# Optimization experiments

Measured on AMD Instinct MI355X. Metric: run time of the kernel, lower is better.

The kernel has to match this reference:

```python
import jax, jax.numpy as jnp
import numpy as np

DN = ('NCHW', 'OIHW', 'NCHW')
BLOB_HW = 16  # hard-coded in make_gaussian_blob_maps

_ENC = [(32, 3), (32, 32), (64, 32), (64, 64), (128, 64), (128, 128), (128, 128)]
_DEC = [(64, 128), (64, 64), (32, 64), (32, 32), (16, 32), (16, 16)]


def _conv(x, w, b, stride):
    y = jax.lax.conv_general_dilated(x, w, (stride, stride), 'SAME', dimension_numbers=DN)
    return y + b[None, :, None, None]


def _tconv(x, w, b):
    # decoder stride-2 stage: 'iteratively doubling the input width'
    y = jax.lax.conv_transpose(x, w, (2, 2), 'SAME', dimension_numbers=DN)
    return y + b[None, :, None, None]


def setup_inputs() -> dict:
    key = jax.random.key(0)
    keys = jax.random.split(key, 1 + 2 * (len(_ENC) + len(_DEC)))
    inp = {'x': jax.random.normal(keys[0], (4, 8, 3, 128, 128), jnp.float32)}
    i = 1
    for j, (o, c) in enumerate(_ENC):
        inp[f'enc_w{j}'] = 0.05 * jax.random.normal(keys[i], (o, c, 3, 3), jnp.float32); i += 1
        inp[f'enc_b{j}'] = 0.05 * jax.random.normal(keys[i], (o,), jnp.float32); i += 1
    for j, (o, c) in enumerate(_DEC):
        inp[f'dec_w{j}'] = 0.05 * jax.random.normal(keys[i], (o, c, 3, 3), jnp.float32); i += 1
        inp[f'dec_b{j}'] = 0.05 * jax.random.normal(keys[i], (o,), jnp.float32); i += 1
    return inp


def _forward(x, enc_w0, enc_b0, enc_w1, enc_b1, enc_w2, enc_b2, enc_w3, enc_b3,
             enc_w4, enc_b4, enc_w5, enc_b5, enc_w6, enc_b6,
             dec_w0, dec_b0, dec_w1, dec_b1, dec_w2, dec_b2,
             dec_w3, dec_b3, dec_w4, dec_b4, dec_w5, dec_b5):
    N, T = x.shape[0], x.shape[1]
    xi = x.reshape((N * T,) + x.shape[2:])  # (B, 3, 128, 128)
    # ---- encoder ----
    h = _conv(xi, enc_w0, enc_b0, 1)                              # Identity act
    h = _conv(h, enc_w1, enc_b1, 1)                               # Identity act
    h = jax.nn.leaky_relu(_conv(h, enc_w2, enc_b2, 2), 0.2)       # 128 -> 64
    h = jax.nn.leaky_relu(_conv(h, enc_w3, enc_b3, 1), 0.2)
    h = jax.nn.leaky_relu(_conv(h, enc_w4, enc_b4, 2), 0.2)       # 64 -> 32
    h = jax.nn.leaky_relu(_conv(h, enc_w5, enc_b5, 1), 0.2)
    R = jax.nn.softplus(_conv(h, enc_w6, enc_b6, 2))              # (B, K, 16, 16)
    B, K, H, W = R.shape
    # ---- keypoint presence: mean over spatial dims ----
    mu = R.sum((2, 3)) / (H * W)                                  # (B, K)
    # ---- normalize_feature_maps: faithful net effect of the in-place loop,
    # which ends up dividing each batch item by the ORIGINAL sum of its LAST map ----
    denom = R[:, K - 1].sum((1, 2))                               # (B,)
    D = R / denom[:, None, None, None]
    # ---- average_feature_maps: spatial-index weighted sum (soft-argmax) ----
    gh = jnp.arange(H, dtype=R.dtype)
    gw = jnp.arange(W, dtype=R.dtype)
    c0 = jnp.einsum('bkhw,h->bk', D, gh)                          # row coord
    c1 = jnp.einsum('bkhw,w->bk', D, gw)                          # col coord
    # ---- gaussian blob maps: mu * exp(-0.5 * ||(u,v) - c||^2), sigma = 1 ----
    u = jnp.arange(BLOB_HW, dtype=R.dtype)[:, None]               # (16, 1)
    v = jnp.arange(BLOB_HW, dtype=R.dtype)[None, :]               # (1, 16)
    d2 = (u[None, None] - c0[:, :, None, None]) ** 2 + (v[None, None] - c1[:, :, None, None]) ** 2
    maps = mu[:, :, None, None] * jnp.exp(-0.5 * d2)              # (B, K, 16, 16)
    # ---- decoder ----
    g = jax.nn.relu(_tconv(maps, dec_w0, dec_b0))                 # 16 -> 32
    g = jax.nn.relu(_conv(g, dec_w1, dec_b1, 1))
    g = jax.nn.relu(_tconv(g, dec_w2, dec_b2))                    # 32 -> 64
    g = jax.nn.relu(_conv(g, dec_w3, dec_b3, 1))
    g = jax.nn.relu(_tconv(g, dec_w4, dec_b4))                    # 64 -> 128
    g = jax.nn.relu(_conv(g, dec_w5, dec_b5, 1))
    return g  # original forward returns the un-reshaped (N*T, C, H, W) tensor


def reference(x, enc_w0, enc_b0, enc_w1, enc_b1, enc_w2, enc_b2, enc_w3, enc_b3,
              enc_w4, enc_b4, enc_w5, enc_b5, enc_w6, enc_b6,
              dec_w0, dec_b0, dec_w1, dec_b1, dec_w2, dec_b2,
              dec_w3, dec_b3, dec_w4, dec_b4, dec_w5, dec_b5):
    return _forward(x, enc_w0, enc_b0, enc_w1, enc_b1, enc_w2, enc_b2, enc_w3, enc_b3,
                    enc_w4, enc_b4, enc_w5, enc_b5, enc_w6, enc_b6,
                    dec_w0, dec_b0, dec_w1, dec_b1, dec_w2, dec_b2,
                    dec_w3, dec_b3, dec_w4, dec_b4, dec_w5, dec_b5)
```

## Files before the change

### kernel.cpp

```cpp
#include <hip/hip_runtime.h>
#include <math.h>


enum { ACT_ID = 0, ACT_LRELU = 1, ACT_SOFTPLUS = 2, ACT_RELU = 3 };

template<int ACT>
__device__ __forceinline__ float act_fn(float x) {
  if (ACT == ACT_LRELU)    return x >= 0.f ? x : 0.2f * x;
  if (ACT == ACT_SOFTPLUS) return fmaxf(x, 0.f) + log1pf(expf(-fabsf(x)));
  if (ACT == ACT_RELU)     return fmaxf(x, 0.f);
  return x;
}

template<int ACT, int NC, int CPT>
__global__ __launch_bounds__(256)
void conv_s1(const float* __restrict__ in, const float* __restrict__ w,
             const float* __restrict__ bias, float* __restrict__ out,
             int Cin, int Cout, int H, int W) {
  const int cogs = Cout / NC;
  const int gx  = blockIdx.x;
  const int cog = gx % cogs;
  const int b   = gx / cogs;
  const int co0 = cog * NC;
  const int Wq  = W / CPT;
  const int items = H * Wq;
  const int item  = blockIdx.y * 256 + threadIdx.x;
  if (item >= items) return;
  const int y  = item / Wq;
  const int x0 = (item - y * Wq) * CPT;

  const int HW = H * W;
  const float* ib = in + (size_t)b * Cin * HW;

  const bool okT = (y > 0), okB = (y < H - 1);
  const bool okL = (x0 > 0), okR = (x0 + CPT < W);
  const int ym = okT ? (y - 1) : 0;
  const int yp = okB ? (y + 1) : 0;
  const int xl = okL ? (x0 - 1) : 0;
  const int xr = okR ? (x0 + CPT) : 0;

  float acc[NC][CPT];
  #pragma unroll
  for (int u = 0; u < NC; ++u)
    #pragma unroll
    for (int q = 0; q < CPT; ++q) acc[u][q] = 0.f;

  for (int ci = 0; ci < Cin; ++ci) {
    const float* p = ib + ci * HW;
    const float* wci = w + ((size_t)co0 * Cin + ci) * 9;
    #pragma unroll
    for (int dy = 0; dy < 3; ++dy) {
      const int  ry    = (dy == 0) ? ym : ((dy == 1) ? y : yp);
      const bool okRow = (dy == 0) ? okT : ((dy == 1) ? true : okB);
      const float* r = p + ry * W;
      float v[CPT + 2];
      if (CPT == 4) {
        float  lf = r[xl];
        float4 m  = *(const float4*)(r + x0);
        float  rf = r[xr];
        v[0] = (okRow && okL) ? lf : 0.f;
        v[1] = okRow ? m.x : 0.f;
        v[2] = okRow ? m.y : 0.f;
        v[3] = okRow ? m.z : 0.f;
        v[4] = okRow ? m.w : 0.f;
        v[5] = (okRow && okR) ? rf : 0.f;
      } else if (CPT == 2) {
        float  lf = r[xl];
        float2 m  = *(const float2*)(r + x0);
        float  rf = r[xr];
        v[0] = (okRow && okL) ? lf : 0.f;
        v[1] = okRow ? m.x : 0.f;
        v[2] = okRow ? m.y : 0.f;
        v[3] = (okRow && okR) ? rf : 0.f;
      } else {
        v[0] = (okRow && okL) ? r[xl] : 0.f;
        #pragma unroll
        for (int q = 0; q < CPT; ++q) v[1 + q] = okRow ? r[x0 + q] : 0.f;
        v[CPT + 1] = (okRow && okR) ? r[xr] : 0.f;
      }
      #pragma unroll
      for (int u = 0; u < NC; ++u) {
        const float* wp = wci + (size_t)u * Cin * 9 + dy * 3;
        const float w0 = wp[0], w1 = wp[1], w2 = wp[2];
        #pragma unroll
        for (int q = 0; q < CPT; ++q)
          acc[u][q] += v[q] * w0 + v[q + 1] * w1 + v[q + 2] * w2;
      }
    }
  }

  #pragma unroll
  for (int u = 0; u < NC; ++u) {
    const float bv = bias[co0 + u];
    float* op = out + ((size_t)(b * Cout + co0 + u) * H + y) * W + x0;
    if (CPT == 4) {
      float4 r4;
      r4.x = act_fn<ACT>(acc[u][0] + bv);
      r4.y = act_fn<ACT>(acc[u][1] + bv);
      r4.z = act_fn<ACT>(acc[u][2] + bv);
      r4.w = act_fn<ACT>(acc[u][3] + bv);
      *(float4*)op = r4;
    } else if (CPT == 2) {
      float2 r2;
      r2.x = act_fn<ACT>(acc[u][0] + bv);
      r2.y = act_fn<ACT>(acc[u][1] + bv);
      *(float2*)op = r2;
    } else {
      #pragma unroll
      for (int q = 0; q < CPT; ++q) op[q] = act_fn<ACT>(acc[u][q] + bv);
    }
  }
}

template<int ACT, int NC, int CPT>
__global__ __launch_bounds__(256)
void conv_s2(const float* __restrict__ in, const float* __restrict__ w,
             const float* __restrict__ bias, float* __restrict__ out,
             int Cin, int Cout, int H, int W) {
  const int Ho = H >> 1, Wo = W >> 1;
  const int cogs = Cout / NC;
  const int gx  = blockIdx.x;
  const int cog = gx % cogs;
  const int b   = gx / cogs;
  const int co0 = cog * NC;
  const int Wq  = Wo / CPT;
  const int items = Ho * Wq;
  const int item  = blockIdx.y * 256 + threadIdx.x;
  if (item >= items) return;
  const int y  = item / Wq;
  const int x0 = (item - y * Wq) * CPT;
  const int ix = 2 * x0;

  const int HW = H * W;
  const float* ib = in + (size_t)b * Cin * HW;

  const int iy0 = 2 * y, iy1 = 2 * y + 1, iy2 = 2 * y + 2;
  const bool okB = (iy2 < H);
  const int iy2c = okB ? iy2 : 0;
  const bool okR = (ix + 2 * CPT < W);
  const int ixr  = okR ? (ix + 2 * CPT) : 0;

  float acc[NC][CPT];
  #pragma unroll
  for (int u = 0; u < NC; ++u)
    #pragma unroll
    for (int q = 0; q < CPT; ++q) acc[u][q] = 0.f;

  for (int ci = 0; ci < Cin; ++ci) {
    const float* p = ib + ci * HW;
    const float* wci = w + ((size_t)co0 * Cin + ci) * 9;
    #pragma unroll
    for (int dy = 0; dy < 3; ++dy) {
      const int  ry    = (dy == 0) ? iy0 : ((dy == 1) ? iy1 : iy2c);
      const bool okRow = (dy < 2) || okB;
      const float* r = p + ry * W;
      float v[2 * CPT + 1];
      if (CPT == 4) {
        float4 m0 = *(const float4*)(r + ix);
        float4 m1 = *(const float4*)(r + ix + 4);
        float  rf = r[ixr];
        v[0] = okRow ? m0.x : 0.f; v[1] = okRow ? m0.y : 0.f;
        v[2] = okRow ? m0.z : 0.f; v[3] = okRow ? m0.w : 0.f;
        v[4] = okRow ? m1.x : 0.f; v[5] = okRow ? m1.y : 0.f;
        v[6] = okRow ? m1.z : 0.f; v[7] = okRow ? m1.w : 0.f;
        v[8] = (okRow && okR) ? rf : 0.f;
      } else if (CPT == 2) {
        float4 m0 = *(const float4*)(r + ix);
        float  rf = r[ixr];
        v[0] = okRow ? m0.x : 0.f; v[1] = okRow ? m0.y : 0.f;
        v[2] = okRow ? m0.z : 0.f; v[3] = okRow ? m0.w : 0.f;
        v[4] = (okRow && okR) ? rf : 0.f;
      } else if (CPT == 1) {
        float2 m0 = *(const float2*)(r + ix);
        float  rf = r[ixr];
        v[0] = okRow ? m0.x : 0.f; v[1] = okRow ? m0.y : 0.f;
        v[2] = (okRow && okR) ? rf : 0.f;
      } else {
        #pragma unroll
        for (int q = 0; q < 2 * CPT; ++q) v[q] = okRow ? r[ix + q] : 0.f;
        v[2 * CPT] = (okRow && okR) ? r[ixr] : 0.f;
      }
      #pragma unroll
      for (int u = 0; u < NC; ++u) {
        const float* wp = wci + (size_t)u * Cin * 9 + dy * 3;
        const float w0 = wp[0], w1 = wp[1], w2 = wp[2];
        #pragma unroll
        for (int q = 0; q < CPT; ++q)
          acc[u][q] += v[2*q] * w0 + v[2*q + 1] * w1 + v[2*q + 2] * w2;
      }
    }
  }

  #pragma unroll
  for (int u = 0; u < NC; ++u) {
    const float bv = bias[co0 + u];
    float* op = out + ((size_t)(b * Cout + co0 + u) * Ho + y) * Wo + x0;
    if (CPT == 4) {
      float4 r4;
      r4.x = act_fn<ACT>(acc[u][0] + bv);
      r4.y = act_fn<ACT>(acc[u][1] + bv);
      r4.z = act_fn<ACT>(acc[u][2] + bv);
      r4.w = act_fn<ACT>(acc[u][3] + bv);
      *(float4*)op = r4;
    } else if (CPT == 2) {
      float2 r2;
      r2.x = act_fn<ACT>(acc[u][0] + bv);
      r2.y = act_fn<ACT>(acc[u][1] + bv);
      *(float2*)op = r2;
    } else {
      #pragma unroll
      for (int q = 0; q < CPT; ++q) op[q] = act_fn<ACT>(acc[u][q] + bv);
    }
  }
}

template<int ACT, int NC>
__global__ __launch_bounds__(256)
void tconv(const float* __restrict__ in, const float* __restrict__ w,
           const float* __restrict__ bias, float* __restrict__ out,
           int Cin, int Cout, int Hin) {
  const int cogs = Cout / NC;
  const int gx  = blockIdx.x;
  const int cog = gx % cogs;
  const int b   = gx / cogs;
  const int co0 = cog * NC;
  const int items = Hin * Hin;
  const int item  = blockIdx.y * 256 + threadIdx.x;
  if (item >= items) return;
  const int i = item / Hin;
  const int j = item - i * Hin;

  const float* ib = in + (size_t)b * Cin * items;
  const bool okT = (i > 0), okL = (j > 0);
  const int im = okT ? i - 1 : 0;
  const int jm = okL ? j - 1 : 0;

  float a00[NC], a01[NC], a10[NC], a11[NC];
  #pragma unroll
  for (int u = 0; u < NC; ++u) { a00[u]=0.f; a01[u]=0.f; a10[u]=0.f; a11[u]=0.f; }

  for (int ci = 0; ci < Cin; ++ci) {
    const float* p = ib + ci * items;
    float xtl = p[im*Hin + jm]; xtl = (okT && okL) ? xtl : 0.f;
    float xtr = p[im*Hin + j];  xtr = okT ? xtr : 0.f;
    float xbl = p[i*Hin + jm];  xbl = okL ? xbl : 0.f;
    float xbr = p[i*Hin + j];
    const float* wci = w + ((size_t)co0 * Cin + ci) * 9;
    #pragma unroll
    for (int u = 0; u < NC; ++u) {
      const float* wp = wci + (size_t)u * Cin * 9;
      const float w00 = wp[0], w01 = wp[1], w02 = wp[2];
      const float w10 = wp[3], w11 = wp[4], w12 = wp[5];
      const float w20 = wp[6], w21 = wp[7], w22 = wp[8];
      a00[u] += xtl*w00 + xtr*w02 + xbl*w20 + xbr*w22;
      a01[u] += xtr*w01 + xbr*w21;
      a10[u] += xbl*w10 + xbr*w12;
      a11[u] += xbr*w11;
    }
  }

  const int Ho = Hin * 2;
  #pragma unroll
  for (int u = 0; u < NC; ++u) {
    const float bv = bias[co0 + u];
    float* op = out + (size_t)(b * Cout + co0 + u) * Ho * Ho + (2*i) * Ho + 2*j;
    float2 t0, t1;
    t0.x = act_fn<ACT>(a00[u] + bv); t0.y = act_fn<ACT>(a01[u] + bv);
    t1.x = act_fn<ACT>(a10[u] + bv); t1.y = act_fn<ACT>(a11[u] + bv);
    *(float2*)op = t0;
    *(float2*)(op + Ho) = t1;
  }
}

__global__ __launch_bounds__(64)
void kp_reduce(const float* __restrict__ R, float* __restrict__ S,
               float* __restrict__ Sh, float* __restrict__ Sw) {
  const int bk = blockIdx.x;
  const int t = threadIdx.x;
  const float* p = R + (size_t)bk * 256;
  float s = 0.f, sh = 0.f, sw = 0.f;
  #pragma unroll
  for (int q = 0; q < 4; ++q) {
    int idx = t + q * 64;
    float v = p[idx];
    s  += v;
    sh += v * (float)(idx >> 4);
    sw += v * (float)(idx & 15);
  }
  #pragma unroll
  for (int off = 32; off > 0; off >>= 1) {
    s  += __shfl_down(s, off);
    sh += __shfl_down(sh, off);
    sw += __shfl_down(sw, off);
  }
  if (t == 0) { S[bk] = s; Sh[bk] = sh; Sw[bk] = sw; }
}

__global__ __launch_bounds__(256)
void kp_maps(const float* __restrict__ S, const float* __restrict__ Sh,
             const float* __restrict__ Sw, float* __restrict__ maps, int K) {
  const int bk = blockIdx.x;
  const int b = bk / K;
  const int t = threadIdx.x;
  const float s   = S[bk];
  const float den = S[b * K + (K - 1)];
  const float mu  = s * (1.0f / 256.0f);
  const float c0  = Sh[bk] / den;
  const float c1  = Sw[bk] / den;
  const float u = (float)(t >> 4);
  const float v = (float)(t & 15);
  const float d2 = (u - c0) * (u - c0) + (v - c1) * (v - c1);
  maps[(size_t)bk * 256 + t] = mu * expf(-0.5f * d2);
}

extern "C" void kernel_launch(void* const* d_in, const int* in_sizes, int n_in,
                              void* d_out, int out_size, void* d_ws, size_t ws_size,
                              hipStream_t stream) {
  const int B = 32;
  const float* x = (const float*)d_in[0];
  const float* ew[7]; const float* eb[7];
  for (int j = 0; j < 7; ++j) { ew[j] = (const float*)d_in[1 + 2*j]; eb[j] = (const float*)d_in[2 + 2*j]; }
  const float* dw[6]; const float* db[6];
  for (int j = 0; j < 6; ++j) { dw[j] = (const float*)d_in[15 + 2*j]; db[j] = (const float*)d_in[16 + 2*j]; }

  float* ws   = (float*)d_ws;
  float* bufA = ws;
  float* bufB = bufA + 16777216;
  float* R    = bufB + 16777216;
  float* maps = R + 1048576;
  float* S    = maps + 1048576;
  float* Sh   = S + 4096;
  float* Sw   = Sh + 4096;
  float* outp = (float*)d_out;

  dim3 blk(256);

  conv_s1<ACT_ID,      8,4><<<dim3(B*4,  16), blk, 0, stream>>>(x,    ew[0], eb[0], bufA, 3,   32,  128, 128);
  conv_s1<ACT_ID,      8,4><<<dim3(B*4,  16), blk, 0, stream>>>(bufA, ew[1], eb[1], bufB, 32,  32,  128, 128);
  conv_s2<ACT_LRELU,   8,4><<<dim3(B*8,   4), blk, 0, stream>>>(bufB, ew[2], eb[2], bufA, 32,  64,  128, 128);
  conv_s1<ACT_LRELU,   8,4><<<dim3(B*8,   4), blk, 0, stream>>>(bufA, ew[3], eb[3], bufB, 64,  64,  64,  64);
  conv_s2<ACT_LRELU,   8,2><<<dim3(B*16,  2), blk, 0, stream>>>(bufB, ew[4], eb[4], bufA, 64,  128, 64,  64);
  conv_s1<ACT_LRELU,   8,2><<<dim3(B*16,  2), blk, 0, stream>>>(bufA, ew[5], eb[5], bufB, 128, 128, 32,  32);
  conv_s2<ACT_SOFTPLUS,4,1><<<dim3(B*32,  1), blk, 0, stream>>>(bufB, ew[6], eb[6], R,    128, 128, 32,  32);

  kp_reduce<<<dim3(B*128), dim3(64), 0, stream>>>(R, S, Sh, Sw);
  kp_maps  <<<dim3(B*128), blk, 0, stream>>>(S, Sh, Sw, maps, 128);

  tconv<ACT_RELU,   2>  <<<dim3(B*32,  1), blk, 0, stream>>>(maps, dw[0], db[0], bufA, 128, 64, 16);
  conv_s1<ACT_RELU, 4,2><<<dim3(B*16,  2), blk, 0, stream>>>(bufA, dw[1], db[1], bufB, 64,  64, 32, 32);
  tconv<ACT_RELU,   4>  <<<dim3(B*8,   4), blk, 0, stream>>>(bufB, dw[2], db[2], bufA, 64,  32, 32);
  conv_s1<ACT_RELU, 8,2><<<dim3(B*4,   8), blk, 0, stream>>>(bufA, dw[3], db[3], bufB, 32,  32, 64, 64);
  tconv<ACT_RELU,   8>  <<<dim3(B*2,  16), blk, 0, stream>>>(bufB, dw[4], db[4], bufA, 32,  16, 64);
  conv_s1<ACT_RELU, 8,4><<<dim3(B*2,  16), blk, 0, stream>>>(bufA, dw[5], db[5], outp, 16,  16, 128, 128);
}
```

Before: 1.267 ms.

## Stage conv weights in shared memory and double-buffer input loads across channels

Each conv, strided conv and transposed-conv block now copies its output-channel weight slice into dynamic shared memory once, so per-channel weights come from LDS rather than repeated global/scalar loads. The channel loop is software-pipelined with two register buffers, so the next channel's input rows load while the current one's FMAs run. conv_s1 also gets a min-blocks-per-CU hint of 4. This costs extra registers for the doubled buffers and a block-wide barrier at kernel start, which may reduce occupancy or cause spills.

```diff
diff --git a/kernel.cpp b/kernel.cpp
--- a/kernel.cpp
+++ b/kernel.cpp
@@ -12,16 +12,80 @@
   return x;
 }
 
+template<int CPT>
+__device__ __forceinline__ void ld_s1(const float* __restrict__ p, int W,
+    int y, int ym, int yp, int xl, int x0, int xr,
+    bool okT, bool okB, bool okL, bool okR, float (&v)[3][CPT + 2]) {
+  #pragma unroll
+  for (int dy = 0; dy < 3; ++dy) {
+    const int  ry    = (dy == 0) ? ym : ((dy == 1) ? y : yp);
+    const bool okRow = (dy == 0) ? okT : ((dy == 1) ? true : okB);
+    const float* r = p + ry * W;
+    if (CPT == 4) {
+      float  lf = r[xl];
+      float4 m  = *(const float4*)(r + x0);
+      float  rf = r[xr];
+      v[dy][0] = (okRow && okL) ? lf : 0.f;
+      v[dy][1] = okRow ? m.x : 0.f;
+      v[dy][2] = okRow ? m.y : 0.f;
+      v[dy][3] = okRow ? m.z : 0.f;
+      v[dy][4] = okRow ? m.w : 0.f;
+      v[dy][5] = (okRow && okR) ? rf : 0.f;
+    } else if (CPT == 2) {
+      float  lf = r[xl];
+      float2 m  = *(const float2*)(r + x0);
+      float  rf = r[xr];
+      v[dy][0] = (okRow && okL) ? lf : 0.f;
+      v[dy][1] = okRow ? m.x : 0.f;
+      v[dy][2] = okRow ? m.y : 0.f;
+      v[dy][3] = (okRow && okR) ? rf : 0.f;
+    } else {
+      v[dy][0] = (okRow && okL) ? r[xl] : 0.f;
+      #pragma unroll
+      for (int q = 0; q < CPT; ++q) v[dy][1 + q] = okRow ? r[x0 + q] : 0.f;
+      v[dy][CPT + 1] = (okRow && okR) ? r[xr] : 0.f;
+    }
+  }
+}
+
+template<int NC, int CPT>
+__device__ __forceinline__ void fma_s1(const float* wl, int Cin, int ci,
+    const float (&v)[3][CPT + 2], float (&acc)[NC][CPT]) {
+  #pragma unroll
+  for (int u = 0; u < NC; ++u) {
+    const float* wp = wl + ((u * Cin + ci) * 9);
+    float wr[9];
+    #pragma unroll
+    for (int k = 0; k < 9; ++k) wr[k] = wp[k];
+    #pragma unroll
+    for (int dy = 0; dy < 3; ++dy)
+      #pragma unroll
+      for (int q = 0; q < CPT; ++q)
+        acc[u][q] += v[dy][q]     * wr[dy * 3]
+                   + v[dy][q + 1] * wr[dy * 3 + 1]
+                   + v[dy][q + 2] * wr[dy * 3 + 2];
+  }
+}
+
 template<int ACT, int NC, int CPT>
-__global__ __launch_bounds__(256)
+__global__ __launch_bounds__(256, 4)
 void conv_s1(const float* __restrict__ in, const float* __restrict__ w,
              const float* __restrict__ bias, float* __restrict__ out,
              int Cin, int Cout, int H, int W) {
+  extern __shared__ float wl[];
   const int cogs = Cout / NC;
   const int gx  = blockIdx.x;
   const int cog = gx % cogs;
   const int b   = gx / cogs;
   const int co0 = cog * NC;
+
+  {
+    const float* wg = w + (size_t)co0 * Cin * 9;
+    const int total = NC * Cin * 9;
+    for (int idx = threadIdx.x; idx < total; idx += 256) wl[idx] = wg[idx];
+  }
+  __syncthreads();
+
   const int Wq  = W / CPT;
   const int items = H * Wq;
   const int item  = blockIdx.y * 256 + threadIdx.x;
@@ -45,49 +109,18 @@
     #pragma unroll
     for (int q = 0; q < CPT; ++q) acc[u][q] = 0.f;
 
-  for (int ci = 0; ci < Cin; ++ci) {
-    const float* p = ib + ci * HW;
-    const float* wci = w + ((size_t)co0 * Cin + ci) * 9;
-    #pragma unroll
-    for (int dy = 0; dy < 3; ++dy) {
-      const int  ry    = (dy == 0) ? ym : ((dy == 1) ? y : yp);
-      const bool okRow = (dy == 0) ? okT : ((dy == 1) ? true : okB);
-      const float* r = p + ry * W;
-      float v[CPT + 2];
-      if (CPT == 4) {
-        float  lf = r[xl];
-        float4 m  = *(const float4*)(r + x0);
-        float  rf = r[xr];
-        v[0] = (okRow && okL) ? lf : 0.f;
-        v[1] = okRow ? m.x : 0.f;
-        v[2] = okRow ? m.y : 0.f;
-        v[3] = okRow ? m.z : 0.f;
-        v[4] = okRow ? m.w : 0.f;
-        v[5] = (okRow && okR) ? rf : 0.f;
-      } else if (CPT == 2) {
-        float  lf = r[xl];
-        float2 m  = *(const float2*)(r + x0);
-        float  rf = r[xr];
-        v[0] = (okRow && okL) ? lf : 0.f;
-        v[1] = okRow ? m.x : 0.f;
-        v[2] = okRow ? m.y : 0.f;
-        v[3] = (okRow && okR) ? rf : 0.f;
-      } else {
-        v[0] = (okRow && okL) ? r[xl] : 0.f;
-        #pragma unroll
-        for (int q = 0; q < CPT; ++q) v[1 + q] = okRow ? r[x0 + q] : 0.f;
-        v[CPT + 1] = (okRow && okR) ? r[xr] : 0.f;
-      }
-      #pragma unroll
-      for (int u = 0; u < NC; ++u) {
-        const float* wp = wci + (size_t)u * Cin * 9 + dy * 3;
-        const float w0 = wp[0], w1 = wp[1], w2 = wp[2];
-        #pragma unroll
-        for (int q = 0; q < CPT; ++q)
-          acc[u][q] += v[q] * w0 + v[q + 1] * w1 + v[q + 2] * w2;
-      }
-    }
-  }
+  float va[3][CPT + 2], vb[3][CPT + 2];
+  ld_s1<CPT>(ib, W, y, ym, yp, xl, x0, xr, okT, okB, okL, okR, va);
+
+  int ci = 0;
+  for (; ci + 2 <= Cin; ci += 2) {
+    ld_s1<CPT>(ib + (size_t)(ci + 1) * HW, W, y, ym, yp, xl, x0, xr, okT, okB, okL, okR, vb);
+    fma_s1<NC, CPT>(wl, Cin, ci, va, acc);
+    if (ci + 2 < Cin)
+      ld_s1<CPT>(ib + (size_t)(ci + 2) * HW, W, y, ym, yp, xl, x0, xr, okT, okB, okL, okR, va);
+    fma_s1<NC, CPT>(wl, Cin, ci + 1, vb, acc);
+  }
+  if (ci < Cin) fma_s1<NC, CPT>(wl, Cin, ci, va, acc);
 
   #pragma unroll
   for (int u = 0; u < NC; ++u) {
@@ -112,17 +145,78 @@
   }
 }
 
+template<int CPT>
+__device__ __forceinline__ void ld_s2(const float* __restrict__ p, int W,
+    int iy0, int iy1, int iy2c, bool okB, int ix, int ixr, bool okR,
+    float (&v)[3][2 * CPT + 1]) {
+  #pragma unroll
+  for (int dy = 0; dy < 3; ++dy) {
+    const int  ry    = (dy == 0) ? iy0 : ((dy == 1) ? iy1 : iy2c);
+    const bool okRow = (dy < 2) || okB;
+    const float* r = p + ry * W;
+    if (CPT == 4) {
+      float4 m0 = *(const float4*)(r + ix);
+      float4 m1 = *(const float4*)(r + ix + 4);
+      float  rf = r[ixr];
+      v[dy][0] = okRow ? m0.x : 0.f; v[dy][1] = okRow ? m0.y : 0.f;
+      v[dy][2] = okRow ? m0.z : 0.f; v[dy][3] = okRow ? m0.w : 0.f;
+      v[dy][4] = okRow ? m1.x : 0.f; v[dy][5] = okRow ? m1.y : 0.f;
+      v[dy][6] = okRow ? m1.z : 0.f; v[dy][7] = okRow ? m1.w : 0.f;
+      v[dy][8] = (okRow && okR) ? rf : 0.f;
+    } else if (CPT == 2) {
+      float4 m0 = *(const float4*)(r + ix);
+      float  rf = r[ixr];
+      v[dy][0] = okRow ? m0.x : 0.f; v[dy][1] = okRow ? m0.y : 0.f;
+      v[dy][2] = okRow ? m0.z : 0.f; v[dy][3] = okRow ? m0.w : 0.f;
+      v[dy][4] = (okRow && okR) ? rf : 0.f;
+    } else {
+      float2 m0 = *(const float2*)(r + ix);
+      float  rf = r[ixr];
+      v[dy][0] = okRow ? m0.x : 0.f; v[dy][1] = okRow ? m0.y : 0.f;
+      v[dy][2] = (okRow && okR) ? rf : 0.f;
+    }
+  }
+}
+
+template<int NC, int CPT>
+__device__ __forceinline__ void fma_s2(const float* wl, int Cin, int ci,
+    const float (&v)[3][2 * CPT + 1], float (&acc)[NC][CPT]) {
+  #pragma unroll
+  for (int u = 0; u < NC; ++u) {
+    const float* wp = wl + ((u * Cin + ci) * 9);
+    float wr[9];
+    #pragma unroll
+    for (int k = 0; k < 9; ++k) wr[k] = wp[k];
+    #pragma unroll
+    for (int dy = 0; dy < 3; ++dy)
+      #pragma unroll
+      for (int q = 0; q < CPT; ++q)
+        acc[u][q] += v[dy][2 * q]     * wr[dy * 3]
+                   + v[dy][2 * q + 1] * wr[dy * 3 + 1]
+                   + v[dy][2 * q + 2] * wr[dy * 3 + 2];
+  }
+}
+
 template<int ACT, int NC, int CPT>
 __global__ __launch_bounds__(256)
 void conv_s2(const float* __restrict__ in, const float* __restrict__ w,
              const float* __restrict__ bias, float* __restrict__ out,
              int Cin, int Cout, int H, int W) {
+  extern __shared__ float wl[];
   const int Ho = H >> 1, Wo = W >> 1;
   const int cogs = Cout / NC;
   const int gx  = blockIdx.x;
   const int cog = gx % cogs;
   const int b   = gx / cogs;
   const int co0 = cog * NC;
+
+  {
+    const float* wg = w + (size_t)co0 * Cin * 9;
+    const int total = NC * Cin * 9;
+    for (int idx = threadIdx.x; idx < total; idx += 256) wl[idx] = wg[idx];
+  }
+  __syncthreads();
+
   const int Wq  = Wo / CPT;
   const int items = Ho * Wq;
   const int item  = blockIdx.y * 256 + threadIdx.x;
@@ -146,50 +240,18 @@
     #pragma unroll
     for (int q = 0; q < CPT; ++q) acc[u][q] = 0.f;
 
-  for (int ci = 0; ci < Cin; ++ci) {
-    const float* p = ib + ci * HW;
-    const float* wci = w + ((size_t)co0 * Cin + ci) * 9;
-    #pragma unroll
-    for (int dy = 0; dy < 3; ++dy) {
-      const int  ry    = (dy == 0) ? iy0 : ((dy == 1) ? iy1 : iy2c);
-      const bool okRow = (dy < 2) || okB;
-      const float* r = p + ry * W;
-      float v[2 * CPT + 1];
-      if (CPT == 4) {
-        float4 m0 = *(const float4*)(r + ix);
-        float4 m1 = *(const float4*)(r + ix + 4);
-        float  rf = r[ixr];
-        v[0] = okRow ? m0.x : 0.f; v[1] = okRow ? m0.y : 0.f;
-        v[2] = okRow ? m0.z : 0.f; v[3] = okRow ? m0.w : 0.f;
-        v[4] = okRow ? m1.x : 0.f; v[5] = okRow ? m1.y : 0.f;
-        v[6] = okRow ? m1.z : 0.f; v[7] = okRow ? m1.w : 0.f;
-        v[8] = (okRow && okR) ? rf : 0.f;
-      } else if (CPT == 2) {
-        float4 m0 = *(const float4*)(r + ix);
-        float  rf = r[ixr];
-        v[0] = okRow ? m0.x : 0.f; v[1] = okRow ? m0.y : 0.f;
-        v[2] = okRow ? m0.z : 0.f; v[3] = okRow ? m0.w : 0.f;
-        v[4] = (okRow && okR) ? rf : 0.f;
-      } else if (CPT == 1) {
-        float2 m0 = *(const float2*)(r + ix);
-        float  rf = r[ixr];
-        v[0] = okRow ? m0.x : 0.f; v[1] = okRow ? m0.y : 0.f;
-        v[2] = (okRow && okR) ? rf : 0.f;
-      } else {
-        #pragma unroll
-        for (int q = 0; q < 2 * CPT; ++q) v[q] = okRow ? r[ix + q] : 0.f;
-        v[2 * CPT] = (okRow && okR) ? r[ixr] : 0.f;
-      }
-      #pragma unroll
-      for (int u = 0; u < NC; ++u) {
-        const float* wp = wci + (size_t)u * Cin * 9 + dy * 3;
-        const float w0 = wp[0], w1 = wp[1], w2 = wp[2];
-        #pragma unroll
-        for (int q = 0; q < CPT; ++q)
-          acc[u][q] += v[2*q] * w0 + v[2*q + 1] * w1 + v[2*q + 2] * w2;
-      }
-    }
-  }
+  float va[3][2 * CPT + 1], vb[3][2 * CPT + 1];
+  ld_s2<CPT>(ib, W, iy0, iy1, iy2c, okB, ix, ixr, okR, va);
+
+  int ci = 0;
+  for (; ci + 2 <= Cin; ci += 2) {
+    ld_s2<CPT>(ib + (size_t)(ci + 1) * HW, W, iy0, iy1, iy2c, okB, ix, ixr, okR, vb);
+    fma_s2<NC, CPT>(wl, Cin, ci, va, acc);
+    if (ci + 2 < Cin)
+      ld_s2<CPT>(ib + (size_t)(ci + 2) * HW, W, iy0, iy1, iy2c, okB, ix, ixr, okR, va);
+    fma_s2<NC, CPT>(wl, Cin, ci + 1, vb, acc);
+  }
+  if (ci < Cin) fma_s2<NC, CPT>(wl, Cin, ci, va, acc);
 
   #pragma unroll
   for (int u = 0; u < NC; ++u) {
@@ -214,16 +276,54 @@
   }
 }
 
+__device__ __forceinline__ void ld_t(const float* __restrict__ p, int Hin,
+    int i, int j, int im, int jm, bool okT, bool okL, float (&xv)[4]) {
+  float xtl = p[im * Hin + jm];
+  float xtr = p[im * Hin + j];
+  float xbl = p[i * Hin + jm];
+  float xbr = p[i * Hin + j];
+  xv[0] = (okT && okL) ? xtl : 0.f;
+  xv[1] = okT ? xtr : 0.f;
+  xv[2] = okL ? xbl : 0.f;
+  xv[3] = xbr;
+}
+
+template<int NC>
+__device__ __forceinline__ void fma_t(const float* wl, int Cin, int ci,
+    const float (&xv)[4],
+    float (&a00)[NC], float (&a01)[NC], float (&a10)[NC], float (&a11)[NC]) {
+  #pragma unroll
+  for (int u = 0; u < NC; ++u) {
+    const float* wp = wl + ((u * Cin + ci) * 9);
+    float wr[9];
+    #pragma unroll
+    for (int k = 0; k < 9; ++k) wr[k] = wp[k];
+    a00[u] += xv[0] * wr[0] + xv[1] * wr[2] + xv[2] * wr[6] + xv[3] * wr[8];
+    a01[u] += xv[1] * wr[1] + xv[3] * wr[7];
+    a10[u] += xv[2] * wr[3] + xv[3] * wr[5];
+    a11[u] += xv[3] * wr[4];
+  }
+}
+
 template<int ACT, int NC>
 __global__ __launch_bounds__(256)
 void tconv(const float* __restrict__ in, const float* __restrict__ w,
            const float* __restrict__ bias, float* __restrict__ out,
            int Cin, int Cout, int Hin) {
+  extern __shared__ float wl[];
   const int cogs = Cout / NC;
   const int gx  = blockIdx.x;
   const int cog = gx % cogs;
   const int b   = gx / cogs;
   const int co0 = cog * NC;
+
+  {
+    const float* wg = w + (size_t)co0 * Cin * 9;
+    const int total = NC * Cin * 9;
+    for (int idx = threadIdx.x; idx < total; idx += 256) wl[idx] = wg[idx];
+  }
+  __syncthreads();
+
   const int items = Hin * Hin;
   const int item  = blockIdx.y * 256 + threadIdx.x;
   if (item >= items) return;
@@ -239,25 +339,18 @@
   #pragma unroll
   for (int u = 0; u < NC; ++u) { a00[u]=0.f; a01[u]=0.f; a10[u]=0.f; a11[u]=0.f; }
 
-  for (int ci = 0; ci < Cin; ++ci) {
-    const float* p = ib + ci * items;
-    float xtl = p[im*Hin + jm]; xtl = (okT && okL) ? xtl : 0.f;
-    float xtr = p[im*Hin + j];  xtr = okT ? xtr : 0.f;
-    float xbl = p[i*Hin + jm];  xbl = okL ? xbl : 0.f;
-    float xbr = p[i*Hin + j];
-    const float* wci = w + ((size_t)co0 * Cin + ci) * 9;
-    #pragma unroll
-    for (int u = 0; u < NC; ++u) {
-      const float* wp = wci + (size_t)u * Cin * 9;
-      const float w00 = wp[0], w01 = wp[1], w02 = wp[2];
-      const float w10 = wp[3], w11 = wp[4], w12 = wp[5];
-      const float w20 = wp[6], w21 = wp[7], w22 = wp[8];
-      a00[u] += xtl*w00 + xtr*w02 + xbl*w20 + xbr*w22;
-      a01[u] += xtr*w01 + xbr*w21;
-      a10[u] += xbl*w10 + xbr*w12;
-      a11[u] += xbr*w11;
-    }
-  }
+  float xa[4], xb[4];
+  ld_t(ib, Hin, i, j, im, jm, okT, okL, xa);
+
+  int ci = 0;
+  for (; ci + 2 <= Cin; ci += 2) {
+    ld_t(ib + (size_t)(ci + 1) * items, Hin, i, j, im, jm, okT, okL, xb);
+    fma_t<NC>(wl, Cin, ci, xa, a00, a01, a10, a11);
+    if (ci + 2 < Cin)
+      ld_t(ib + (size_t)(ci + 2) * items, Hin, i, j, im, jm, okT, okL, xa);
+    fma_t<NC>(wl, Cin, ci + 1, xb, a00, a01, a10, a11);
+  }
+  if (ci < Cin) fma_t<NC>(wl, Cin, ci, xa, a00, a01, a10, a11);
 
   const int Ho = Hin * 2;
   #pragma unroll
@@ -334,22 +427,24 @@
   float* outp = (float*)d_out;
 
   dim3 blk(256);
-
-  conv_s1<ACT_ID,      8,4><<<dim3(B*4,  16), blk, 0, stream>>>(x,    ew[0], eb[0], bufA, 3,   32,  128, 128);
-  conv_s1<ACT_ID,      8,4><<<dim3(B*4,  16), blk, 0, stream>>>(bufA, ew[1], eb[1], bufB, 32,  32,  128, 128);
-  conv_s2<ACT_LRELU,   8,4><<<dim3(B*8,   4), blk, 0, stream>>>(bufB, ew[2], eb[2], bufA, 32,  64,  128, 128);
-  conv_s1<ACT_LRELU,   8,4><<<dim3(B*8,   4), blk, 0, stream>>>(bufA, ew[3], eb[3], bufB, 64,  64,  64,  64);
-  conv_s2<ACT_LRELU,   8,2><<<dim3(B*16,  2), blk, 0, stream>>>(bufB, ew[4], eb[4], bufA, 64,  128, 64,  64);
-  conv_s1<ACT_LRELU,   8,2><<<dim3(B*16,  2), blk, 0, stream>>>(bufA, ew[5], eb[5], bufB, 128, 128, 32,  32);
-  conv_s2<ACT_SOFTPLUS,4,1><<<dim3(B*32,  1), blk, 0, stream>>>(bufB, ew[6], eb[6], R,    128, 128, 32,  32);
+  #define WSZ(NC, CIN) ((NC) * (CIN) * 9 * (int)sizeof(float))
+
+  conv_s1<ACT_ID,      8,4><<<dim3(B*4,  16), blk, WSZ(8,3),   stream>>>(x,    ew[0], eb[0], bufA, 3,   32,  128, 128);
+  conv_s1<ACT_ID,      8,4><<<dim3(B*4,  16), blk, WSZ(8,32),  stream>>>(bufA, ew[1], eb[1], bufB, 32,  32,  128, 128);
+  conv_s2<ACT_LRELU,   8,4><<<dim3(B*8,   4), blk, WSZ(8,32),  stream>>>(bufB, ew[2], eb[2], bufA, 32,  64,  128, 128);
+  conv_s1<ACT_LRELU,   8,4><<<dim3(B*8,   4), blk, WSZ(8,64),  stream>>>(bufA, ew[3], eb[3], bufB, 64,  64,  64,  64);
+  conv_s2<ACT_LRELU,   8,2><<<dim3(B*16,  2), blk, WSZ(8,64),  stream>>>(bufB, ew[4], eb[4], bufA, 64,  128, 64,  64);
+  conv_s1<ACT_LRELU,   8,2><<<dim3(B*16,  2), blk, WSZ(8,128), stream>>>(bufA, ew[5], eb[5], bufB, 128, 128, 32,  32);
+  conv_s2<ACT_SOFTPLUS,4,1><<<dim3(B*32,  1), blk, WSZ(4,128), stream>>>(bufB, ew[6], eb[6], R,    128, 128, 32,  32);
 
   kp_reduce<<<dim3(B*128), dim3(64), 0, stream>>>(R, S, Sh, Sw);
   kp_maps  <<<dim3(B*128), blk, 0, stream>>>(S, Sh, Sw, maps, 128);
 
-  tconv<ACT_RELU,   2>  <<<dim3(B*32,  1), blk, 0, stream>>>(maps, dw[0], db[0], bufA, 128, 64, 16);
-  conv_s1<ACT_RELU, 4,2><<<dim3(B*16,  2), blk, 0, stream>>>(bufA, dw[1], db[1], bufB, 64,  64, 32, 32);
-  tconv<ACT_RELU,   4>  <<<dim3(B*8,   4), blk, 0, stream>>>(bufB, dw[2], db[2], bufA, 64,  32, 32);
-  conv_s1<ACT_RELU, 8,2><<<dim3(B*4,   8), blk, 0, stream>>>(bufA, dw[3], db[3], bufB, 32,  32, 64, 64);
-  tconv<ACT_RELU,   8>  <<<dim3(B*2,  16), blk, 0, stream>>>(bufB, dw[4], db[4], bufA, 32,  16, 64);
-  conv_s1<ACT_RELU, 8,4><<<dim3(B*2,  16), blk, 0, stream>>>(bufA, dw[5], db[5], outp, 16,  16, 128, 128);
-}
+  tconv<ACT_RELU,   2>  <<<dim3(B*32,  1), blk, WSZ(2,128), stream>>>(maps, dw[0], db[0], bufA, 128, 64, 16);
+  conv_s1<ACT_RELU, 4,2><<<dim3(B*16,  2), blk, WSZ(4,64),  stream>>>(bufA, dw[1], db[1], bufB, 64,  64, 32, 32);
+  tconv<ACT_RELU,   4>  <<<dim3(B*8,   4), blk, WSZ(4,64),  stream>>>(bufB, dw[2], db[2], bufA, 64,  32, 32);
+  conv_s1<ACT_RELU, 8,2><<<dim3(B*4,   8), blk, WSZ(8,32),  stream>>>(bufA, dw[3], db[3], bufB, 32,  32, 64, 64);
+  tconv<ACT_RELU,   8>  <<<dim3(B*2,  16), blk, WSZ(8,32),  stream>>>(bufB, dw[4], db[4], bufA, 32,  16, 64);
+  conv_s1<ACT_RELU, 8,4><<<dim3(B*2,  16), blk, WSZ(8,16),  stream>>>(bufA, dw[5], db[5], outp, 16,  16, 128, 128);
+  #undef WSZ
+}
```

Result: slower. 4.070 ms (+221.2%).
